# Performance work log

Hardware: AMD Instinct MI355X
Metric: run time of the kernel (lower is better)

The kernel has to match this reference:

```python
import jax, jax.numpy as jnp
import numpy as np

N = 500_000        # nodes
F = 128            # node feature dim
E = 4_000_000      # edges
B = 4              # graphs in batch
COORD_RANGE = 256.0
VOXEL = 8.0        # voxel_size (same per dim, from init size=[8,8,8])
G = int(COORD_RANGE // VOXEL)   # 32 voxels per dim
V = B * G * G * G               # fixed number of voxel slots
EFFECTIVE_RADIUS = 8.0          # Cartesian max_value


def setup_inputs() -> dict:
    key = jax.random.key(0)
    k1, k2, k3 = jax.random.split(key, 3)
    x = jax.random.normal(k1, (N, F), dtype=jnp.float32)
    pos = jax.random.uniform(k2, (N, 3), dtype=jnp.float32) * COORD_RANGE
    # sorted segment ids: B contiguous graphs
    batch = ((jnp.arange(N) * B) // N).astype(jnp.int32)
    edge_index = jax.random.randint(k3, (2, E), 0, N, dtype=jnp.int64)
    return {"x": x, "pos": pos, "batch": batch, "edge_index": edge_index}


def reference(x, pos, batch, edge_index):
    # ---- voxel_grid: assign each node to a (batch, voxel) cluster ----
    v = jnp.clip(jnp.floor(pos / VOXEL).astype(jnp.int32), 0, G - 1)  # [N,3]
    vid = batch * (G * G * G) + v[:, 0] * (G * G) + v[:, 1] * G + v[:, 2]  # [N]

    # ---- max_pool: scatter-max features, mean positions per cluster ----
    pooled_x = jax.ops.segment_max(x, vid, num_segments=V)            # [V,F]
    count = jax.ops.segment_sum(jnp.ones((N,), x.dtype), vid, num_segments=V)  # [V]
    occupied = count > 0
    pooled_x = jnp.where(occupied[:, None], pooled_x, 0.0)
    pooled_pos = jax.ops.segment_sum(pos, vid, num_segments=V) / jnp.maximum(count, 1.0)[:, None]  # [V,3]

    # ---- remap edges to clusters; mask self-loops (coalesce approximated by mask) ----
    src = vid[edge_index[0]]  # [E]
    dst = vid[edge_index[1]]  # [E]
    edge_mask = src != dst
    new_edge_index = jnp.stack([src, dst])  # [2,E]

    # ---- Cartesian(cat=False, norm=True, max_value=effective_radius) ----
    cart = pooled_pos[dst] - pooled_pos[src]                 # [E,3]
    edge_attr = cart / (2.0 * EFFECTIVE_RADIUS) + 0.5
    edge_attr = jnp.where(edge_mask[:, None], edge_attr, 0.0)

    return pooled_x, pooled_pos, new_edge_index, edge_attr, edge_mask
```

## Files before the change

### kernel.cpp

```cpp
#include <hip/hip_runtime.h>

#define NN 500000
#define FF 128
#define EE 4000000
#define BB 4
#define GG 32
#define VV (BB * GG * GG * GG)

#define OUT_X    0
#define OUT_POS  (VV * FF)
#define OUT_EIDX (OUT_POS + VV * 3)
#define OUT_ATTR (OUT_EIDX + 2 * EE)
#define OUT_MASK (OUT_ATTR + 3 * EE)

__global__ __launch_bounds__(256) void vid_kernel(
    const float* __restrict__ pos, const int* __restrict__ batch,
    int* __restrict__ vid, unsigned int* __restrict__ cnt)
{
    int n = blockIdx.x * 256 + threadIdx.x;
    if (n >= NN) return;
    float px = pos[3 * n + 0], py = pos[3 * n + 1], pz = pos[3 * n + 2];
    int vx = min(max((int)floorf(px * 0.125f), 0), GG - 1);
    int vy = min(max((int)floorf(py * 0.125f), 0), GG - 1);
    int vz = min(max((int)floorf(pz * 0.125f), 0), GG - 1);
    int v = batch[n] * (GG * GG * GG) + vx * (GG * GG) + vy * GG + vz;
    vid[n] = v;
    atomicAdd(&cnt[v], 1u);
}

__global__ __launch_bounds__(256) void scan_local_kernel(
    const unsigned int* __restrict__ cnt, unsigned int* __restrict__ offs,
    unsigned int* __restrict__ bsum)
{
    __shared__ unsigned int s[256];
    int i = blockIdx.x * 256 + threadIdx.x;
    unsigned int val = cnt[i];
    s[threadIdx.x] = val;
    __syncthreads();
    for (int d = 1; d < 256; d <<= 1) {
        unsigned int t = (threadIdx.x >= d) ? s[threadIdx.x - d] : 0u;
        __syncthreads();
        s[threadIdx.x] += t;
        __syncthreads();
    }
    offs[i] = s[threadIdx.x] - val;
    if (threadIdx.x == 255) bsum[blockIdx.x] = s[255];
}

__global__ __launch_bounds__(512) void scan_bsum_kernel(unsigned int* __restrict__ bsum)
{
    __shared__ unsigned int s[512];
    unsigned int val = bsum[threadIdx.x];
    s[threadIdx.x] = val;
    __syncthreads();
    for (int d = 1; d < 512; d <<= 1) {
        unsigned int t = (threadIdx.x >= d) ? s[threadIdx.x - d] : 0u;
        __syncthreads();
        s[threadIdx.x] += t;
        __syncthreads();
    }
    bsum[threadIdx.x] = s[threadIdx.x] - val;
}

__global__ __launch_bounds__(256) void scan_add_kernel(
    const unsigned int* __restrict__ offs_in, const unsigned int* __restrict__ bsum,
    const unsigned int* __restrict__ cnt,
    unsigned int* __restrict__ cursor, uint2* __restrict__ meta)
{
    int i = blockIdx.x * 256 + threadIdx.x;
    unsigned int o = offs_in[i] + bsum[blockIdx.x];
    cursor[i] = o;
    meta[i] = make_uint2(o, cnt[i]);
}

__global__ __launch_bounds__(256) void scatter_kernel(
    const int* __restrict__ vid, unsigned int* __restrict__ cursor,
    unsigned int* __restrict__ order)
{
    int n = blockIdx.x * 256 + threadIdx.x;
    if (n >= NN) return;
    unsigned int p = atomicAdd(&cursor[vid[n]], 1u);
    order[p] = n;
}

__global__ __launch_bounds__(256) void pool_kernel(
    const float* __restrict__ x, const float* __restrict__ pos,
    const unsigned int* __restrict__ order, const uint2* __restrict__ meta,
    float* __restrict__ out_x, float* __restrict__ out_pos,
    float4* __restrict__ pos4)
{
    int w = threadIdx.x >> 6;
    int lane = threadIdx.x & 63;
    int g = lane >> 4;
    int fl = lane & 15;
    int v = blockIdx.x * 4 + w;
    uint2 mt = meta[v];
    unsigned int start = mt.x;
    unsigned int c = mt.y;

    float4 mlo = make_float4(-INFINITY, -INFINITY, -INFINITY, -INFINITY);
    float4 mhi = mlo;
    float sx = 0.0f, sy = 0.0f, sz = 0.0f;

    for (unsigned int base = 0; base < c; base += 64) {
        unsigned int rem = min(c - base, 64u);
        unsigned int idx = (lane < rem) ? order[start + base + lane] : 0u;
        if (lane < rem) {
            const float* pp = pos + 3 * (size_t)idx;
            sx += pp[0]; sy += pp[1]; sz += pp[2];
        }
        for (unsigned int k = (unsigned int)g; k < rem; k += 4) {
            unsigned int n = __shfl(idx, (int)k);
            const float4* row = (const float4*)(x + (size_t)n * FF);
            float4 a = row[fl];
            float4 b = row[fl + 16];
            mlo.x = fmaxf(mlo.x, a.x); mlo.y = fmaxf(mlo.y, a.y);
            mlo.z = fmaxf(mlo.z, a.z); mlo.w = fmaxf(mlo.w, a.w);
            mhi.x = fmaxf(mhi.x, b.x); mhi.y = fmaxf(mhi.y, b.y);
            mhi.z = fmaxf(mhi.z, b.z); mhi.w = fmaxf(mhi.w, b.w);
        }
    }

    #define MERGE(f) f = fmaxf(f, __shfl_xor(f, 16)); f = fmaxf(f, __shfl_xor(f, 32));
    MERGE(mlo.x) MERGE(mlo.y) MERGE(mlo.z) MERGE(mlo.w)
    MERGE(mhi.x) MERGE(mhi.y) MERGE(mhi.z) MERGE(mhi.w)
    #undef MERGE

    float4 res = (lane < 16) ? mlo : mhi;
    if (c == 0) res = make_float4(0.0f, 0.0f, 0.0f, 0.0f);
    if (lane < 32)
        ((float4*)(out_x + (size_t)v * FF))[lane] = res;

    for (int d = 1; d < 64; d <<= 1) {
        sx += __shfl_xor(sx, d);
        sy += __shfl_xor(sy, d);
        sz += __shfl_xor(sz, d);
    }
    if (lane == 0) {
        float inv = 1.0f / fmaxf((float)c, 1.0f);
        float mx = sx * inv, my = sy * inv, mz = sz * inv;
        out_pos[3 * v + 0] = mx;
        out_pos[3 * v + 1] = my;
        out_pos[3 * v + 2] = mz;
        pos4[v] = make_float4(mx, my, mz, 0.0f);
    }
}

__global__ __launch_bounds__(256) void edge_kernel(
    const int* __restrict__ eidx, const int* __restrict__ vid,
    const float4* __restrict__ pos4, float* __restrict__ out)
{
    __shared__ float sattr[1536];
    int t = threadIdx.x;
    size_t e0 = (size_t)blockIdx.x * 512;
    int rem = (int)((EE - e0 < 512) ? (EE - e0) : 512);
    size_t p = e0 / 2 + t;
    float a0x = 0.f, a0y = 0.f, a0z = 0.f, a1x = 0.f, a1y = 0.f, a1z = 0.f;
    if (2 * t < rem) {
        int2 s2 = ((const int2*)eidx)[p];
        int2 d2 = ((const int2*)(eidx + EE))[p];
        int sv0 = vid[s2.x], sv1 = vid[s2.y];
        int dv0 = vid[d2.x], dv1 = vid[d2.y];
        bool m0 = (sv0 != dv0), m1 = (sv1 != dv1);
        ((float2*)(out + OUT_EIDX))[p]      = make_float2((float)sv0, (float)sv1);
        ((float2*)(out + OUT_EIDX + EE))[p] = make_float2((float)dv0, (float)dv1);
        ((float2*)(out + OUT_MASK))[p]      = make_float2(m0 ? 1.f : 0.f, m1 ? 1.f : 0.f);
        if (m0) {
            float4 ps = pos4[sv0], pd = pos4[dv0];
            a0x = (pd.x - ps.x) * 0.0625f + 0.5f;
            a0y = (pd.y - ps.y) * 0.0625f + 0.5f;
            a0z = (pd.z - ps.z) * 0.0625f + 0.5f;
        }
        if (m1) {
            float4 ps = pos4[sv1], pd = pos4[dv1];
            a1x = (pd.x - ps.x) * 0.0625f + 0.5f;
            a1y = (pd.y - ps.y) * 0.0625f + 0.5f;
            a1z = (pd.z - ps.z) * 0.0625f + 0.5f;
        }
    }
    sattr[6 * t + 0] = a0x; sattr[6 * t + 1] = a0y; sattr[6 * t + 2] = a0z;
    sattr[6 * t + 3] = a1x; sattr[6 * t + 4] = a1y; sattr[6 * t + 5] = a1z;
    __syncthreads();
    float2* dst = (float2*)(out + OUT_ATTR + 3 * e0);
    const float2* sp = (const float2*)sattr;
    int nf2 = 3 * rem / 2;
    #pragma unroll
    for (int i = 0; i < 3; ++i) {
        int idx = i * 256 + t;
        if (idx < nf2) dst[idx] = sp[idx];
    }
}

extern "C" void kernel_launch(void* const* d_in, const int* in_sizes, int n_in,
                              void* d_out, int out_size, void* d_ws, size_t ws_size,
                              hipStream_t stream)
{
    const float* x     = (const float*)d_in[0];
    const float* pos   = (const float*)d_in[1];
    const int*   batch = (const int*)d_in[2];
    const int*   eidx  = (const int*)d_in[3];
    float* out = (float*)d_out;

    char* ws = (char*)d_ws;
    unsigned int* cnt     = (unsigned int*)(ws + 0);
    int*          vid     = (int*)(ws + 524288);
    unsigned int* offs    = (unsigned int*)(ws + 2524288);
    unsigned int* cursor  = (unsigned int*)(ws + 3048576);
    unsigned int* bsum    = (unsigned int*)(ws + 3572864);
    unsigned int* order   = (unsigned int*)(ws + 3574912);
    uint2*        meta    = (uint2*)(ws + 5574912);
    float4*       pos4    = (float4*)(ws + 6623488);

    hipMemsetAsync(d_ws, 0, 524288, stream);

    vid_kernel<<<(NN + 255) / 256, 256, 0, stream>>>(pos, batch, vid, cnt);
    scan_local_kernel<<<VV / 256, 256, 0, stream>>>(cnt, offs, bsum);
    scan_bsum_kernel<<<1, 512, 0, stream>>>(bsum);
    scan_add_kernel<<<VV / 256, 256, 0, stream>>>(offs, bsum, cnt, cursor, meta);
    scatter_kernel<<<(NN + 255) / 256, 256, 0, stream>>>(vid, cursor, order);
    pool_kernel<<<VV / 4, 256, 0, stream>>>(x, pos, order, meta,
                                            out + OUT_X, out + OUT_POS, pos4);
    edge_kernel<<<(EE + 511) / 512, 256, 0, stream>>>(eidx, vid, pos4, out);
}
```

Measured before the change: 557.3 us.

## Write per-node pooled record to cut edge gathers; vectorize and fuse scan

The pool kernel now writes a per-node float4 record (cluster mean position plus the cluster id stored as a float), so the edge kernel does a single dependent gather per endpoint instead of a vid lookup followed by a pos4 lookup. The edge kernel handles four edges per thread with int4/float4 loads and stores. The vid and scatter kernels handle four nodes per thread, and the block-sum scan is fused into the add pass by having each block re-reduce the preceding bsum entries. The trade-offs are an extra scattered write of 500K 16-byte records, an exact-float comparison of cluster ids (safe since ids stay below 2^24), and redundant prefix-sum work in every scan block.

Measured after the change: 557.7 us. About the same (+0.1%).

```diff
diff --git a/kernel.cpp b/kernel.cpp
--- a/kernel.cpp
+++ b/kernel.cpp
@@ -14,18 +14,28 @@
 #define OUT_MASK (OUT_ATTR + 3 * EE)
 
 __global__ __launch_bounds__(256) void vid_kernel(
-    const float* __restrict__ pos, const int* __restrict__ batch,
-    int* __restrict__ vid, unsigned int* __restrict__ cnt)
-{
-    int n = blockIdx.x * 256 + threadIdx.x;
-    if (n >= NN) return;
-    float px = pos[3 * n + 0], py = pos[3 * n + 1], pz = pos[3 * n + 2];
-    int vx = min(max((int)floorf(px * 0.125f), 0), GG - 1);
-    int vy = min(max((int)floorf(py * 0.125f), 0), GG - 1);
-    int vz = min(max((int)floorf(pz * 0.125f), 0), GG - 1);
-    int v = batch[n] * (GG * GG * GG) + vx * (GG * GG) + vy * GG + vz;
-    vid[n] = v;
-    atomicAdd(&cnt[v], 1u);
+    const float4* __restrict__ posv, const int4* __restrict__ batch4,
+    int4* __restrict__ vid4, unsigned int* __restrict__ cnt)
+{
+    int q = blockIdx.x * 256 + threadIdx.x;
+    if (q >= NN / 4) return;
+    float4 p0 = posv[3 * q], p1 = posv[3 * q + 1], p2 = posv[3 * q + 2];
+    int4 b = batch4[q];
+    auto vox = [](float px, float py, float pz, int bb) {
+        int vx = min(max((int)floorf(px * 0.125f), 0), GG - 1);
+        int vy = min(max((int)floorf(py * 0.125f), 0), GG - 1);
+        int vz = min(max((int)floorf(pz * 0.125f), 0), GG - 1);
+        return bb * (GG * GG * GG) + vx * (GG * GG) + vy * GG + vz;
+    };
+    int v0 = vox(p0.x, p0.y, p0.z, b.x);
+    int v1 = vox(p0.w, p1.x, p1.y, b.y);
+    int v2 = vox(p1.z, p1.w, p2.x, b.z);
+    int v3 = vox(p2.y, p2.z, p2.w, b.w);
+    vid4[q] = make_int4(v0, v1, v2, v3);
+    atomicAdd(&cnt[v0], 1u);
+    atomicAdd(&cnt[v1], 1u);
+    atomicAdd(&cnt[v2], 1u);
+    atomicAdd(&cnt[v3], 1u);
 }
 
 __global__ __launch_bounds__(256) void scan_local_kernel(
@@ -47,47 +57,44 @@
     if (threadIdx.x == 255) bsum[blockIdx.x] = s[255];
 }
 
-__global__ __launch_bounds__(512) void scan_bsum_kernel(unsigned int* __restrict__ bsum)
-{
-    __shared__ unsigned int s[512];
-    unsigned int val = bsum[threadIdx.x];
-    s[threadIdx.x] = val;
-    __syncthreads();
-    for (int d = 1; d < 512; d <<= 1) {
-        unsigned int t = (threadIdx.x >= d) ? s[threadIdx.x - d] : 0u;
-        __syncthreads();
-        s[threadIdx.x] += t;
-        __syncthreads();
-    }
-    bsum[threadIdx.x] = s[threadIdx.x] - val;
-}
-
-__global__ __launch_bounds__(256) void scan_add_kernel(
-    const unsigned int* __restrict__ offs_in, const unsigned int* __restrict__ bsum,
+__global__ __launch_bounds__(256) void scan_fuse_kernel(
+    const unsigned int* __restrict__ offs_local, const unsigned int* __restrict__ bsum,
     const unsigned int* __restrict__ cnt,
     unsigned int* __restrict__ cursor, uint2* __restrict__ meta)
 {
-    int i = blockIdx.x * 256 + threadIdx.x;
-    unsigned int o = offs_in[i] + bsum[blockIdx.x];
+    __shared__ unsigned int red[4];
+    int t = threadIdx.x;
+    unsigned int partial = 0;
+    for (int i = t; i < blockIdx.x; i += 256) partial += bsum[i];
+    for (int d = 1; d < 64; d <<= 1) partial += __shfl_xor(partial, d);
+    if ((t & 63) == 0) red[t >> 6] = partial;
+    __syncthreads();
+    unsigned int prefix = red[0] + red[1] + red[2] + red[3];
+    int i = blockIdx.x * 256 + t;
+    unsigned int o = offs_local[i] + prefix;
     cursor[i] = o;
     meta[i] = make_uint2(o, cnt[i]);
 }
 
 __global__ __launch_bounds__(256) void scatter_kernel(
-    const int* __restrict__ vid, unsigned int* __restrict__ cursor,
+    const int4* __restrict__ vid4, unsigned int* __restrict__ cursor,
     unsigned int* __restrict__ order)
 {
-    int n = blockIdx.x * 256 + threadIdx.x;
-    if (n >= NN) return;
-    unsigned int p = atomicAdd(&cursor[vid[n]], 1u);
-    order[p] = n;
+    int q = blockIdx.x * 256 + threadIdx.x;
+    if (q >= NN / 4) return;
+    int4 v = vid4[q];
+    unsigned int n = 4u * (unsigned int)q;
+    order[atomicAdd(&cursor[v.x], 1u)] = n;
+    order[atomicAdd(&cursor[v.y], 1u)] = n + 1;
+    order[atomicAdd(&cursor[v.z], 1u)] = n + 2;
+    order[atomicAdd(&cursor[v.w], 1u)] = n + 3;
 }
 
 __global__ __launch_bounds__(256) void pool_kernel(
     const float* __restrict__ x, const float* __restrict__ pos,
     const unsigned int* __restrict__ order, const uint2* __restrict__ meta,
     float* __restrict__ out_x, float* __restrict__ out_pos,
-    float4* __restrict__ pos4)
+    float4* __restrict__ node_rec)
 {
     int w = threadIdx.x >> 6;
     int lane = threadIdx.x & 63;
@@ -101,10 +108,12 @@
     float4 mlo = make_float4(-INFINITY, -INFINITY, -INFINITY, -INFINITY);
     float4 mhi = mlo;
     float sx = 0.0f, sy = 0.0f, sz = 0.0f;
+    unsigned int my_idx = 0u;
 
     for (unsigned int base = 0; base < c; base += 64) {
         unsigned int rem = min(c - base, 64u);
         unsigned int idx = (lane < rem) ? order[start + base + lane] : 0u;
+        my_idx = idx;
         if (lane < rem) {
             const float* pp = pos + 3 * (size_t)idx;
             sx += pp[0]; sy += pp[1]; sz += pp[2];
@@ -136,59 +145,63 @@
         sy += __shfl_xor(sy, d);
         sz += __shfl_xor(sz, d);
     }
+    float inv = 1.0f / fmaxf((float)c, 1.0f);
+    float mx = sx * inv, my = sy * inv, mz = sz * inv;
     if (lane == 0) {
-        float inv = 1.0f / fmaxf((float)c, 1.0f);
-        float mx = sx * inv, my = sy * inv, mz = sz * inv;
         out_pos[3 * v + 0] = mx;
         out_pos[3 * v + 1] = my;
         out_pos[3 * v + 2] = mz;
-        pos4[v] = make_float4(mx, my, mz, 0.0f);
+    }
+    float4 recv = make_float4(mx, my, mz, (float)v);
+    if (c <= 64) {
+        if (lane < (int)c) node_rec[my_idx] = recv;
+    } else {
+        for (unsigned int base = 0; base < c; base += 64) {
+            unsigned int rem = min(c - base, 64u);
+            if (lane < rem) node_rec[order[start + base + lane]] = recv;
+        }
     }
 }
 
 __global__ __launch_bounds__(256) void edge_kernel(
-    const int* __restrict__ eidx, const int* __restrict__ vid,
-    const float4* __restrict__ pos4, float* __restrict__ out)
-{
-    __shared__ float sattr[1536];
+    const int4* __restrict__ esrc4, const int4* __restrict__ edst4,
+    const float4* __restrict__ rec, float* __restrict__ out)
+{
+    __shared__ float sattr[3072];
     int t = threadIdx.x;
-    size_t e0 = (size_t)blockIdx.x * 512;
-    int rem = (int)((EE - e0 < 512) ? (EE - e0) : 512);
-    size_t p = e0 / 2 + t;
-    float a0x = 0.f, a0y = 0.f, a0z = 0.f, a1x = 0.f, a1y = 0.f, a1z = 0.f;
-    if (2 * t < rem) {
-        int2 s2 = ((const int2*)eidx)[p];
-        int2 d2 = ((const int2*)(eidx + EE))[p];
-        int sv0 = vid[s2.x], sv1 = vid[s2.y];
-        int dv0 = vid[d2.x], dv1 = vid[d2.y];
-        bool m0 = (sv0 != dv0), m1 = (sv1 != dv1);
-        ((float2*)(out + OUT_EIDX))[p]      = make_float2((float)sv0, (float)sv1);
-        ((float2*)(out + OUT_EIDX + EE))[p] = make_float2((float)dv0, (float)dv1);
-        ((float2*)(out + OUT_MASK))[p]      = make_float2(m0 ? 1.f : 0.f, m1 ? 1.f : 0.f);
-        if (m0) {
-            float4 ps = pos4[sv0], pd = pos4[dv0];
-            a0x = (pd.x - ps.x) * 0.0625f + 0.5f;
-            a0y = (pd.y - ps.y) * 0.0625f + 0.5f;
-            a0z = (pd.z - ps.z) * 0.0625f + 0.5f;
-        }
-        if (m1) {
-            float4 ps = pos4[sv1], pd = pos4[dv1];
-            a1x = (pd.x - ps.x) * 0.0625f + 0.5f;
-            a1y = (pd.y - ps.y) * 0.0625f + 0.5f;
-            a1z = (pd.z - ps.z) * 0.0625f + 0.5f;
-        }
-    }
-    sattr[6 * t + 0] = a0x; sattr[6 * t + 1] = a0y; sattr[6 * t + 2] = a0z;
-    sattr[6 * t + 3] = a1x; sattr[6 * t + 4] = a1y; sattr[6 * t + 5] = a1z;
+    size_t e0 = (size_t)blockIdx.x * 1024;
+    int rem = (int)(((size_t)EE - e0 < 1024) ? ((size_t)EE - e0) : 1024);
+    size_t q = e0 / 4 + t;
+    if (4 * t < rem) {
+        int4 s = esrc4[q];
+        int4 d = edst4[q];
+        float4 rs0 = rec[s.x], rs1 = rec[s.y], rs2 = rec[s.z], rs3 = rec[s.w];
+        float4 rd0 = rec[d.x], rd1 = rec[d.y], rd2 = rec[d.z], rd3 = rec[d.w];
+        bool m0 = (rs0.w != rd0.w), m1 = (rs1.w != rd1.w);
+        bool m2 = (rs2.w != rd2.w), m3 = (rs3.w != rd3.w);
+        ((float4*)(out + OUT_EIDX))[q]      = make_float4(rs0.w, rs1.w, rs2.w, rs3.w);
+        ((float4*)(out + OUT_EIDX + EE))[q] = make_float4(rd0.w, rd1.w, rd2.w, rd3.w);
+        ((float4*)(out + OUT_MASK))[q]      = make_float4(m0 ? 1.f : 0.f, m1 ? 1.f : 0.f,
+                                                          m2 ? 1.f : 0.f, m3 ? 1.f : 0.f);
+        float* sa = sattr + 12 * t;
+        sa[0]  = m0 ? (rd0.x - rs0.x) * 0.0625f + 0.5f : 0.f;
+        sa[1]  = m0 ? (rd0.y - rs0.y) * 0.0625f + 0.5f : 0.f;
+        sa[2]  = m0 ? (rd0.z - rs0.z) * 0.0625f + 0.5f : 0.f;
+        sa[3]  = m1 ? (rd1.x - rs1.x) * 0.0625f + 0.5f : 0.f;
+        sa[4]  = m1 ? (rd1.y - rs1.y) * 0.0625f + 0.5f : 0.f;
+        sa[5]  = m1 ? (rd1.z - rs1.z) * 0.0625f + 0.5f : 0.f;
+        sa[6]  = m2 ? (rd2.x - rs2.x) * 0.0625f + 0.5f : 0.f;
+        sa[7]  = m2 ? (rd2.y - rs2.y) * 0.0625f + 0.5f : 0.f;
+        sa[8]  = m2 ? (rd2.z - rs2.z) * 0.0625f + 0.5f : 0.f;
+        sa[9]  = m3 ? (rd3.x - rs3.x) * 0.0625f + 0.5f : 0.f;
+        sa[10] = m3 ? (rd3.y - rs3.y) * 0.0625f + 0.5f : 0.f;
+        sa[11] = m3 ? (rd3.z - rs3.z) * 0.0625f + 0.5f : 0.f;
+    }
     __syncthreads();
-    float2* dst = (float2*)(out + OUT_ATTR + 3 * e0);
-    const float2* sp = (const float2*)sattr;
-    int nf2 = 3 * rem / 2;
-    #pragma unroll
-    for (int i = 0; i < 3; ++i) {
-        int idx = i * 256 + t;
-        if (idx < nf2) dst[idx] = sp[idx];
-    }
+    float4* dst = (float4*)(out + OUT_ATTR + 3 * e0);
+    const float4* sp = (const float4*)sattr;
+    int nf4 = 3 * rem / 4;
+    for (int i = t; i < nf4; i += 256) dst[i] = sp[i];
 }
 
 extern "C" void kernel_launch(void* const* d_in, const int* in_sizes, int n_in,
@@ -202,23 +215,25 @@
     float* out = (float*)d_out;
 
     char* ws = (char*)d_ws;
-    unsigned int* cnt     = (unsigned int*)(ws + 0);
-    int*          vid     = (int*)(ws + 524288);
-    unsigned int* offs    = (unsigned int*)(ws + 2524288);
-    unsigned int* cursor  = (unsigned int*)(ws + 3048576);
-    unsigned int* bsum    = (unsigned int*)(ws + 3572864);
-    unsigned int* order   = (unsigned int*)(ws + 3574912);
-    uint2*        meta    = (uint2*)(ws + 5574912);
-    float4*       pos4    = (float4*)(ws + 6623488);
+    unsigned int* cnt      = (unsigned int*)(ws + 0);
+    int*          vid      = (int*)(ws + 524288);
+    unsigned int* offs     = (unsigned int*)(ws + 2524288);
+    unsigned int* cursor   = (unsigned int*)(ws + 3048576);
+    unsigned int* bsum     = (unsigned int*)(ws + 3572864);
+    unsigned int* order    = (unsigned int*)(ws + 3574912);
+    uint2*        meta     = (uint2*)(ws + 5574912);
+    float4*       node_rec = (float4*)(ws + 6623488);
 
     hipMemsetAsync(d_ws, 0, 524288, stream);
 
-    vid_kernel<<<(NN + 255) / 256, 256, 0, stream>>>(pos, batch, vid, cnt);
+    vid_kernel<<<(NN / 4 + 255) / 256, 256, 0, stream>>>(
+        (const float4*)pos, (const int4*)batch, (int4*)vid, cnt);
     scan_local_kernel<<<VV / 256, 256, 0, stream>>>(cnt, offs, bsum);
-    scan_bsum_kernel<<<1, 512, 0, stream>>>(bsum);
-    scan_add_kernel<<<VV / 256, 256, 0, stream>>>(offs, bsum, cnt, cursor, meta);
-    scatter_kernel<<<(NN + 255) / 256, 256, 0, stream>>>(vid, cursor, order);
+    scan_fuse_kernel<<<VV / 256, 256, 0, stream>>>(offs, bsum, cnt, cursor, meta);
+    scatter_kernel<<<(NN / 4 + 255) / 256, 256, 0, stream>>>(
+        (const int4*)vid, cursor, order);
     pool_kernel<<<VV / 4, 256, 0, stream>>>(x, pos, order, meta,
-                                            out + OUT_X, out + OUT_POS, pos4);
-    edge_kernel<<<(EE + 511) / 512, 256, 0, stream>>>(eidx, vid, pos4, out);
-}
+                                            out + OUT_X, out + OUT_POS, node_rec);
+    edge_kernel<<<(EE + 1023) / 1024, 256, 0, stream>>>(
+        (const int4*)eidx, (const int4*)(eidx + EE), node_rec, out);
+}
```
